# Optimization experiments

Measured on AMD Instinct MI355X. Metric: run time of the kernel, lower is better.

## Reference

```python
import jax, jax.numpy as jnp
import numpy as np

D = 1024      # input_size
H = 16        # num_heads
HD = D // H   # head_dim
B, S = 8, 1024


def setup_inputs() -> dict:
    key = jax.random.key(0)
    ks = jax.random.split(key, 9)
    s = 1.0 / np.sqrt(D)
    return {
        "x": jax.random.normal(ks[0], (B, S, D), dtype=jnp.float32),
        "Wq": jax.random.uniform(ks[1], (D, D), jnp.float32, -s, s),
        "bq": jax.random.uniform(ks[2], (D,), jnp.float32, -s, s),
        "Wk": jax.random.uniform(ks[3], (D, D), jnp.float32, -s, s),
        "bk": jax.random.uniform(ks[4], (D,), jnp.float32, -s, s),
        "Wv": jax.random.uniform(ks[5], (D, D), jnp.float32, -s, s),
        "bv": jax.random.uniform(ks[6], (D,), jnp.float32, -s, s),
        "Wf": jax.random.uniform(ks[7], (D, D), jnp.float32, -s, s),
        "bf": jax.random.uniform(ks[8], (D,), jnp.float32, -s, s),
    }


def reference(x, Wq, bq, Wk, bk, Wv, bv, Wf, bf):
    b, s, d = x.shape
    # torch Linear: x @ W.T + b; split into heads -> [b, H, s, HD]
    def split(y):
        return y.reshape(b, s, H, HD).transpose(0, 2, 1, 3)
    q = split(x @ Wq.T + bq)
    k = split(x @ Wk.T + bk)
    v = split(x @ Wv.T + bv)
    scores = jnp.einsum("bhqd,bhkd->bhqk", q, k) / jnp.sqrt(jnp.float32(HD))
    probs = jax.nn.softmax(scores, axis=-1)
    ctx = jnp.einsum("bhqk,bhkd->bhqd", probs, v)
    ctx = ctx.transpose(0, 2, 1, 3).reshape(b, s, d)
    out = ctx @ Wf.T + bf
    return (out, probs)
```

## Files before the change

kernel.cpp:

```cpp
#include <hip/hip_runtime.h>

typedef __bf16 bf16;
typedef __bf16 bf16x4 __attribute__((ext_vector_type(4)));
typedef __bf16 bf16x8 __attribute__((ext_vector_type(8)));
typedef float  f32x4  __attribute__((ext_vector_type(4)));

constexpr int Bb = 8, Ss = 1024, Dd = 1024, Hh = 16, HDd = 64;
constexpr int Mm = Bb * Ss;
constexpr int Kk = 1024;

struct CastArgs {
  const float* src[5];
  bf16* dst[5];
  int cum[5];
};
__global__ void cast_all(CastArgs a, int tot) {
  int i = blockIdx.x * blockDim.x + threadIdx.x;
  if (i >= tot) return;
  int s, base;
  if (i < a.cum[0])      { s = 0; base = 0; }
  else if (i < a.cum[1]) { s = 1; base = a.cum[0]; }
  else if (i < a.cum[2]) { s = 2; base = a.cum[1]; }
  else if (i < a.cum[3]) { s = 3; base = a.cum[2]; }
  else                   { s = 4; base = a.cum[3]; }
  int j = i - base;
  float4 v = reinterpret_cast<const float4*>(a.src[s])[j];
  bf16x4 o = { (bf16)v.x, (bf16)v.y, (bf16)v.z, (bf16)v.w };
  reinterpret_cast<bf16x4*>(a.dst[s])[j] = o;
}

__device__ __forceinline__ void gemm_loop(const bf16* __restrict__ A, const bf16* __restrict__ Bm,
                                          int bm, int bn, unsigned char* As, unsigned char* Bs,
                                          int w, int lane, int l15, int g, f32x4 (&acc)[4][4]) {
  const bf16* srcA[4];
  const bf16* srcB[4];
#pragma unroll
  for (int i = 0; i < 4; ++i) {
    int gch = (w * 4 + i) * 64 + lane;
    int r = gch >> 3, c = gch & 7, cs = c ^ (r & 7);
    srcA[i] = A  + (size_t)(bm * 128 + r) * Kk + cs * 8;
    srcB[i] = Bm + (size_t)(bn * 128 + r) * Kk + cs * 8;
  }
  for (int kt = 0; kt < Kk / 64; ++kt) {
    __syncthreads();
#pragma unroll
    for (int i = 0; i < 4; ++i) {
      __builtin_amdgcn_global_load_lds(
          (const __attribute__((address_space(1))) void*)(srcA[i] + kt * 64),
          (__attribute__((address_space(3))) void*)(As + (w * 4 + i) * 1024), 16, 0, 0);
      __builtin_amdgcn_global_load_lds(
          (const __attribute__((address_space(1))) void*)(srcB[i] + kt * 64),
          (__attribute__((address_space(3))) void*)(Bs + (w * 4 + i) * 1024), 16, 0, 0);
    }
    __syncthreads();
#pragma unroll
    for (int kk = 0; kk < 2; ++kk) {
      const int kb = kk * 64 + g * 16;
      bf16x8 af[4], bfr[4];
#pragma unroll
      for (int mi = 0; mi < 4; ++mi) {
        int row = ((w >> 1) * 64) + mi * 16 + l15;
        af[mi] = *reinterpret_cast<const bf16x8*>(As + row * 128 + (kb ^ ((row & 7) << 4)));
      }
#pragma unroll
      for (int ni = 0; ni < 4; ++ni) {
        int row = ((w & 1) * 64) + ni * 16 + l15;
        bfr[ni] = *reinterpret_cast<const bf16x8*>(Bs + row * 128 + (kb ^ ((row & 7) << 4)));
      }
#pragma unroll
      for (int mi = 0; mi < 4; ++mi)
#pragma unroll
        for (int ni = 0; ni < 4; ++ni)
          acc[mi][ni] = __builtin_amdgcn_mfma_f32_16x16x32_bf16(af[mi], bfr[ni], acc[mi][ni], 0, 0, 0);
    }
  }
}

__global__ __launch_bounds__(256) void gemm_qkv(const bf16* __restrict__ x,
                                                const bf16* __restrict__ wq, const bf16* __restrict__ wk,
                                                const bf16* __restrict__ wv,
                                                const float* __restrict__ bq, const float* __restrict__ bk,
                                                const float* __restrict__ bv,
                                                bf16* __restrict__ Qo, bf16* __restrict__ Ko,
                                                bf16* __restrict__ Vto) {
  const int tid = threadIdx.x;
  const int lane = tid & 63;
  const int w = tid >> 6;
  const int l15 = lane & 15, g = lane >> 4;
  const int z = blockIdx.z;

  const bf16* A; const bf16* Bm; int bm, bn;
  if (z < 2) { A = x; Bm = z ? wk : wq; bm = blockIdx.x; bn = blockIdx.y; }
  else       { A = wv; Bm = x;          bm = blockIdx.y; bn = blockIdx.x; }

  __shared__ __align__(16) unsigned char As[128 * 128];
  __shared__ __align__(16) unsigned char Bs[128 * 128];
  f32x4 acc[4][4] = {};
  gemm_loop(A, Bm, bm, bn, As, Bs, w, lane, l15, g, acc);

  const int wr = (w >> 1) * 64, wc = (w & 1) * 64;
  if (z < 2) {
    const float* bias = z ? bk : bq;
    bf16* out = z ? Ko : Qo;
    const float scale = z ? 1.f : 0.125f;
#pragma unroll
    for (int ni = 0; ni < 4; ++ni) {
      int col = bn * 128 + wc + ni * 16 + l15;
      float bv_ = bias[col];
#pragma unroll
      for (int mi = 0; mi < 4; ++mi)
#pragma unroll
        for (int r = 0; r < 4; ++r) {
          int row = bm * 128 + wr + mi * 16 + g * 4 + r;
          float val = (acc[mi][ni][r] + bv_) * scale;
          size_t adr = ((size_t)((row >> 10) * Hh + (col >> 6)) * Ss + (row & 1023)) * HDd + (col & 63);
          out[adr] = (bf16)val;
        }
    }
  } else {
#pragma unroll
    for (int mi = 0; mi < 4; ++mi)
#pragma unroll
      for (int r = 0; r < 4; ++r) {
        int row = bm * 128 + wr + mi * 16 + g * 4 + r;
        float bv_ = bv[row];
#pragma unroll
        for (int ni = 0; ni < 4; ++ni) {
          int col = bn * 128 + wc + ni * 16 + l15;
          size_t adr = ((size_t)((col >> 10) * Hh + (row >> 6)) * HDd + (row & 63)) * Ss + (col & 1023);
          Vto[adr] = (bf16)(acc[mi][ni][r] + bv_);
        }
      }
  }
}

__global__ __launch_bounds__(256) void gemm_out(const bf16* __restrict__ A, const bf16* __restrict__ Bm,
                                                const float* __restrict__ bias, float* __restrict__ out) {
  const int tid = threadIdx.x;
  const int lane = tid & 63;
  const int w = tid >> 6;
  const int l15 = lane & 15, g = lane >> 4;
  const int bn = blockIdx.x, bm = blockIdx.y;
  __shared__ __align__(16) unsigned char As[128 * 128];
  __shared__ __align__(16) unsigned char Bs[128 * 128];
  f32x4 acc[4][4] = {};
  gemm_loop(A, Bm, bm, bn, As, Bs, w, lane, l15, g, acc);
  const int wr = (w >> 1) * 64, wc = (w & 1) * 64;
#pragma unroll
  for (int ni = 0; ni < 4; ++ni) {
    int col = bn * 128 + wc + ni * 16 + l15;
    float bv_ = bias[col];
#pragma unroll
    for (int mi = 0; mi < 4; ++mi)
#pragma unroll
      for (int r = 0; r < 4; ++r) {
        int row = bm * 128 + wr + mi * 16 + g * 4 + r;
        out[(size_t)row * Dd + col] = acc[mi][ni][r] + bv_;
      }
  }
}

__global__ __launch_bounds__(512, 4) void attn_fused(const bf16* __restrict__ Q,
                                                     const bf16* __restrict__ Kt,
                                                     const bf16* __restrict__ Vt,
                                                     float* __restrict__ probs,
                                                     bf16* __restrict__ ctx) {
  const int tid = threadIdx.x;
  const int lane = tid & 63;
  const int w = tid >> 6;
  const int l15 = lane & 15, g = lane >> 4;
  const int bid = blockIdx.x;
  const int bh = (bid & 7) * 16 + ((bid >> 3) & 15);
  const int qt = bid >> 7;
  const int q0 = qt * 128 + w * 16;

  __shared__ __align__(16) unsigned char KV[4][16384];
  __shared__ __align__(16) bf16 Ps[8][16][40];

  bf16x8 qf0, qf1;
  {
    const bf16* qp = Q + ((size_t)bh * Ss + q0 + l15) * HDd + g * 8;
    qf0 = *reinterpret_cast<const bf16x8*>(qp);
    qf1 = *reinterpret_cast<const bf16x8*>(qp + 32);
  }
  const bf16* kbase = Kt + (size_t)bh * Ss * HDd;
  const bf16* vbase = Vt + (size_t)bh * HDd * Ss;

  const bf16* ksrc[2];
  const bf16* vsrc[2];
#pragma unroll
  for (int i = 0; i < 2; ++i) {
    int ch = i * 512 + tid;
    int kr = ch >> 3, kc = (ch & 7) ^ (kr & 7);
    ksrc[i] = kbase + (size_t)kr * HDd + kc * 8;
    int vr = ch >> 4, vc = (ch & 15) ^ (vr & 15);
    vsrc[i] = vbase + (size_t)vr * Ss + vc * 8;
  }

#define SK(slab, t)                                                                       \
  {                                                                                       \
    _Pragma("unroll") for (int i = 0; i < 2; ++i)                                         \
        __builtin_amdgcn_global_load_lds(                                                 \
            (const __attribute__((address_space(1))) void*)(ksrc[i] + (size_t)(t) * 128 * HDd), \
            (__attribute__((address_space(3))) void*)(KV[slab] + (i * 512 + w * 64) * 16),\
            16, 0, 0);                                                                    \
  }
#define SV(slab, t)                                                                       \
  {                                                                                       \
    _Pragma("unroll") for (int i = 0; i < 2; ++i)                                         \
        __builtin_amdgcn_global_load_lds(                                                 \
            (const __attribute__((address_space(1))) void*)(vsrc[i] + (t) * 128),         \
            (__attribute__((address_space(3))) void*)(KV[slab] + (i * 512 + w * 64) * 16),\
            16, 0, 0);                                                                    \
  }

  auto kread = [&](int slab, int nk, int half) -> bf16x8 {
    int row = nk * 16 + l15;
    int chunk = (half * 4 + g) ^ (l15 & 7);
    return *reinterpret_cast<const bf16x8*>(KV[slab] + row * 128 + chunk * 16);
  };
  auto vread = [&](int slab, int nkp, int ni) -> bf16x8 {
    int row = ni * 16 + l15;
    int chunk = (nkp * 4 + g) ^ l15;
    return *reinterpret_cast<const bf16x8*>(KV[slab] + row * 256 + chunk * 16);
  };

  float lr0 = 0.f, lr1 = 0.f, lr2 = 0.f, lr3 = 0.f;
  SK(0, 0);
  __syncthreads();
  for (int kt = 0; kt < 8; ++kt) {
    if (kt < 7) { SK((kt + 1) & 1, kt + 1); }
    else        { SK(0, 0); SV(2, 0); }
    const int ks = kt & 1;
#pragma unroll
    for (int nk = 0; nk < 8; ++nk) {
      f32x4 sc = {0.f, 0.f, 0.f, 0.f};
      sc = __builtin_amdgcn_mfma_f32_16x16x32_bf16(kread(ks, nk, 0), qf0, sc, 0, 0, 0);
      sc = __builtin_amdgcn_mfma_f32_16x16x32_bf16(kread(ks, nk, 1), qf1, sc, 0, 0, 0);
      lr0 += __expf(sc[0]); lr1 += __expf(sc[1]);
      lr2 += __expf(sc[2]); lr3 += __expf(sc[3]);
    }
    __syncthreads();
  }
  float lsum = (lr0 + lr1) + (lr2 + lr3);
  lsum += __shfl_xor(lsum, 16, 64);
  lsum += __shfl_xor(lsum, 32, 64);
  const float rl = 1.f / lsum;

  float* const prow = probs + ((size_t)bh * Ss + q0 + l15) * Ss;
  f32x4 cacc[4] = {};

  for (int kt = 0; kt < 8; ++kt) {
    if (kt < 7) { SK((kt + 1) & 1, kt + 1); SV(2 + ((kt + 1) & 1), kt + 1); }
    const int ks = kt & 1, vs = 2 + (kt & 1);
#pragma unroll
    for (int nkp = 0; nkp < 4; ++nkp) {
#pragma unroll
      for (int h = 0; h < 2; ++h) {
        int nk = nkp * 2 + h;
        f32x4 sc = {0.f, 0.f, 0.f, 0.f};
        sc = __builtin_amdgcn_mfma_f32_16x16x32_bf16(kread(ks, nk, 0), qf0, sc, 0, 0, 0);
        sc = __builtin_amdgcn_mfma_f32_16x16x32_bf16(kread(ks, nk, 1), qf1, sc, 0, 0, 0);
        f32x4 pv;
#pragma unroll
        for (int r = 0; r < 4; ++r) pv[r] = __expf(sc[r]) * rl;
        *reinterpret_cast<f32x4*>(prow + kt * 128 + nk * 16 + g * 4) = pv;
        bf16x4 pb = { (bf16)pv[0], (bf16)pv[1], (bf16)pv[2], (bf16)pv[3] };
        *reinterpret_cast<bf16x4*>(&Ps[w][l15][h * 16 + g * 4]) = pb;
      }
      bf16x8 pf = *reinterpret_cast<const bf16x8*>(&Ps[w][l15][g * 8]);
#pragma unroll
      for (int ni = 0; ni < 4; ++ni)
        cacc[ni] = __builtin_amdgcn_mfma_f32_16x16x32_bf16(pf, vread(vs, nkp, ni), cacc[ni], 0, 0, 0);
    }
    __syncthreads();
  }
#undef SK
#undef SV

  const int bb = bh >> 4, hh = bh & 15;
#pragma unroll
  for (int ni = 0; ni < 4; ++ni)
#pragma unroll
    for (int r = 0; r < 4; ++r) {
      int q = q0 + g * 4 + r;
      ctx[((size_t)bb * Ss + q) * Dd + hh * 64 + ni * 16 + l15] = (bf16)cacc[ni][r];
    }
}

extern "C" void kernel_launch(void* const* d_in, const int* in_sizes, int n_in,
                              void* d_out, int out_size, void* d_ws, size_t ws_size,
                              hipStream_t stream) {
  (void)in_sizes; (void)n_in; (void)out_size; (void)ws_size;
  const float* x   = (const float*)d_in[0];
  const float* Wq  = (const float*)d_in[1];
  const float* bq  = (const float*)d_in[2];
  const float* Wk  = (const float*)d_in[3];
  const float* bk  = (const float*)d_in[4];
  const float* Wv  = (const float*)d_in[5];
  const float* bv  = (const float*)d_in[6];
  const float* Wf  = (const float*)d_in[7];
  const float* bfp = (const float*)d_in[8];

  char* ws = (char*)d_ws;
  size_t off = 0;
  auto alloc = [&](size_t n) { void* p = ws + off; off += (n + 255) & ~(size_t)255; return p; };
  bf16* xb   = (bf16*)alloc((size_t)Mm * Dd * 2);
  bf16* wqb  = (bf16*)alloc((size_t)Dd * Dd * 2);
  bf16* wkb  = (bf16*)alloc((size_t)Dd * Dd * 2);
  bf16* wvb  = (bf16*)alloc((size_t)Dd * Dd * 2);
  bf16* wfb  = (bf16*)alloc((size_t)Dd * Dd * 2);
  bf16* Qb   = (bf16*)alloc((size_t)Mm * Dd * 2);
  bf16* Kb   = (bf16*)alloc((size_t)Mm * Dd * 2);
  bf16* Vtb  = (bf16*)alloc((size_t)Mm * Dd * 2);
  bf16* ctxb = (bf16*)alloc((size_t)Mm * Dd * 2);

  CastArgs ca;
  ca.src[0] = x;  ca.dst[0] = xb;  int n0 = Mm * Dd / 4;
  ca.src[1] = Wq; ca.dst[1] = wqb; int nw = Dd * Dd / 4;
  ca.src[2] = Wk; ca.dst[2] = wkb;
  ca.src[3] = Wv; ca.dst[3] = wvb;
  ca.src[4] = Wf; ca.dst[4] = wfb;
  ca.cum[0] = n0; ca.cum[1] = n0 + nw; ca.cum[2] = n0 + 2 * nw;
  ca.cum[3] = n0 + 3 * nw; ca.cum[4] = n0 + 4 * nw;
  int tot = ca.cum[4];
  cast_all<<<(tot + 255) / 256, 256, 0, stream>>>(ca, tot);

  gemm_qkv<<<dim3(Mm / 128, Dd / 128, 3), 256, 0, stream>>>(xb, wqb, wkb, wvb, bq, bk, bv, Qb, Kb, Vtb);

  float* probs = (float*)d_out + (size_t)Mm * Dd;
  attn_fused<<<dim3(Bb * Hh * 8), 512, 0, stream>>>(Qb, Kb, Vtb, probs, ctxb);

  gemm_out<<<dim3(Dd / 128, Mm / 128), 256, 0, stream>>>(ctxb, wfb, bfp, (float*)d_out);
}
```

Measured before the change: 264.1 us.

## Deepen K prefetch pipeline and use explicit vmcnt waits with MFMA priority

In the first (row-sum) pass, the attention kernel now uses all four LDS slabs as a 4-deep ring for K tiles, prefetching three tiles ahead instead of double-buffering. It replaces __syncthreads with explicit s_waitcnt vmcnt counts plus a raw barrier, so loads still in flight are not drained at every step. It also groups LDS fragment reads ahead of the MFMAs and raises wave priority around the MFMA instructions. The aim is to hide global-to-LDS latency and keep the matrix units busy. The cost is fragile hand-counted vmcnt values and sched barriers that constrain compiler scheduling, so a wrong count could cause a data race.

```diff
diff --git a/kernel.cpp b/kernel.cpp
--- a/kernel.cpp
+++ b/kernel.cpp
@@ -160,6 +160,9 @@
   }
 }
 
+#define WAITV(n) asm volatile("s_waitcnt vmcnt(" #n ")" ::: "memory")
+#define PHASE_BAR { __builtin_amdgcn_s_barrier(); __builtin_amdgcn_sched_barrier(0); }
+
 __global__ __launch_bounds__(512, 4) void attn_fused(const bf16* __restrict__ Q,
                                                      const bf16* __restrict__ Kt,
                                                      const bf16* __restrict__ Vt,
@@ -226,21 +229,30 @@
   };
 
   float lr0 = 0.f, lr1 = 0.f, lr2 = 0.f, lr3 = 0.f;
-  SK(0, 0);
-  __syncthreads();
+  SK(0, 0); SK(1, 1); SK(2, 2);
+  __builtin_amdgcn_sched_barrier(0);
+  WAITV(4);
+  PHASE_BAR;
   for (int kt = 0; kt < 8; ++kt) {
-    if (kt < 7) { SK((kt + 1) & 1, kt + 1); }
-    else        { SK(0, 0); SV(2, 0); }
-    const int ks = kt & 1;
+    if (kt <= 4)      { SK((kt + 3) & 3, kt + 3); }
+    else if (kt == 7) { SK(0, 0); SV(2, 0); }
+    __builtin_amdgcn_sched_barrier(0);
+    const int ks = kt & 3;
 #pragma unroll
     for (int nk = 0; nk < 8; ++nk) {
       f32x4 sc = {0.f, 0.f, 0.f, 0.f};
-      sc = __builtin_amdgcn_mfma_f32_16x16x32_bf16(kread(ks, nk, 0), qf0, sc, 0, 0, 0);
-      sc = __builtin_amdgcn_mfma_f32_16x16x32_bf16(kread(ks, nk, 1), qf1, sc, 0, 0, 0);
+      bf16x8 k0 = kread(ks, nk, 0), k1 = kread(ks, nk, 1);
+      __builtin_amdgcn_s_setprio(1);
+      sc = __builtin_amdgcn_mfma_f32_16x16x32_bf16(k0, qf0, sc, 0, 0, 0);
+      sc = __builtin_amdgcn_mfma_f32_16x16x32_bf16(k1, qf1, sc, 0, 0, 0);
+      __builtin_amdgcn_s_setprio(0);
       lr0 += __expf(sc[0]); lr1 += __expf(sc[1]);
       lr2 += __expf(sc[2]); lr3 += __expf(sc[3]);
     }
-    __syncthreads();
+    if (kt <= 4)      { WAITV(4); }
+    else if (kt == 5) { WAITV(2); }
+    else              { WAITV(0); }
+    PHASE_BAR;
   }
   float lsum = (lr0 + lr1) + (lr2 + lr3);
   lsum += __shfl_xor(lsum, 16, 64);
@@ -252,6 +264,7 @@
 
   for (int kt = 0; kt < 8; ++kt) {
     if (kt < 7) { SK((kt + 1) & 1, kt + 1); SV(2 + ((kt + 1) & 1), kt + 1); }
+    __builtin_amdgcn_sched_barrier(0);
     const int ks = kt & 1, vs = 2 + (kt & 1);
 #pragma unroll
     for (int nkp = 0; nkp < 4; ++nkp) {
@@ -259,8 +272,11 @@
       for (int h = 0; h < 2; ++h) {
         int nk = nkp * 2 + h;
         f32x4 sc = {0.f, 0.f, 0.f, 0.f};
-        sc = __builtin_amdgcn_mfma_f32_16x16x32_bf16(kread(ks, nk, 0), qf0, sc, 0, 0, 0);
-        sc = __builtin_amdgcn_mfma_f32_16x16x32_bf16(kread(ks, nk, 1), qf1, sc, 0, 0, 0);
+        bf16x8 k0 = kread(ks, nk, 0), k1 = kread(ks, nk, 1);
+        __builtin_amdgcn_s_setprio(1);
+        sc = __builtin_amdgcn_mfma_f32_16x16x32_bf16(k0, qf0, sc, 0, 0, 0);
+        sc = __builtin_amdgcn_mfma_f32_16x16x32_bf16(k1, qf1, sc, 0, 0, 0);
+        __builtin_amdgcn_s_setprio(0);
         f32x4 pv;
 #pragma unroll
         for (int r = 0; r < 4; ++r) pv[r] = __expf(sc[r]) * rl;
@@ -269,11 +285,19 @@
         *reinterpret_cast<bf16x4*>(&Ps[w][l15][h * 16 + g * 4]) = pb;
       }
       bf16x8 pf = *reinterpret_cast<const bf16x8*>(&Ps[w][l15][g * 8]);
-#pragma unroll
-      for (int ni = 0; ni < 4; ++ni)
-        cacc[ni] = __builtin_amdgcn_mfma_f32_16x16x32_bf16(pf, vread(vs, nkp, ni), cacc[ni], 0, 0, 0);
-    }
-    __syncthreads();
+      bf16x8 vf0 = vread(vs, nkp, 0), vf1 = vread(vs, nkp, 1);
+      bf16x8 vf2 = vread(vs, nkp, 2), vf3 = vread(vs, nkp, 3);
+      __builtin_amdgcn_s_setprio(1);
+      cacc[0] = __builtin_amdgcn_mfma_f32_16x16x32_bf16(pf, vf0, cacc[0], 0, 0, 0);
+      cacc[1] = __builtin_amdgcn_mfma_f32_16x16x32_bf16(pf, vf1, cacc[1], 0, 0, 0);
+      cacc[2] = __builtin_amdgcn_mfma_f32_16x16x32_bf16(pf, vf2, cacc[2], 0, 0, 0);
+      cacc[3] = __builtin_amdgcn_mfma_f32_16x16x32_bf16(pf, vf3, cacc[3], 0, 0, 0);
+      __builtin_amdgcn_s_setprio(0);
+    }
+    if (kt < 7) {
+      WAITV(8);
+      PHASE_BAR;
+    }
   }
 #undef SK
 #undef SV
```

Result: no change. 263.8 us (-0.1%).
